# Optimization experiments

Hardware: AMD Instinct MI355X
Metric: run time of the kernel (lower is better)

## Reference

```python
import jax, jax.numpy as jnp
import numpy as np
from jax import lax

B = 16
DEPTH = 24
D_MODEL = 192
D_INNER = 384   # expand=2
D_STATE = 16
D_CONV = 4
DT_RANK = 12    # ceil(192/16)
PATCH = 16
EPS = 1e-5


def setup_inputs() -> dict:
    key = jax.random.key(0)
    ks = jax.random.split(key, 24)
    def n(k, shape, s):
        return jax.random.normal(k, shape, jnp.float32) * s
    inp = {}
    inp["x_img"] = jax.random.normal(ks[0], (B, 3, 256, 256), jnp.float32)
    inp["z_img"] = jax.random.normal(ks[1], (B, 3, 128, 128), jnp.float32)
    # patch embed conv
    inp["patch_w"] = n(ks[2], (D_MODEL, 3, PATCH, PATCH), 0.02)
    inp["patch_b"] = jnp.zeros((D_MODEL,), jnp.float32)
    # abs pos embeds (token counts fixed by module: 256 for x, 64 for z)
    inp["pos_x"] = n(ks[3], (1, 256, D_MODEL), 0.02)
    inp["pos_z"] = n(ks[4], (1, 64, D_MODEL), 0.02)
    # per-layer norms (LayerNorm, rms_norm=False)
    inp["ln_w"] = jnp.ones((DEPTH, D_MODEL), jnp.float32)
    inp["ln_b"] = jnp.zeros((DEPTH, D_MODEL), jnp.float32)
    # Mamba mixer params (stacked over depth)
    inp["in_w"] = n(ks[5], (DEPTH, 2 * D_INNER, D_MODEL), 0.05)          # in_proj (no bias)
    inp["conv_w"] = n(ks[6], (DEPTH, D_INNER, D_CONV), 0.2)              # depthwise conv1d
    inp["conv_b"] = jnp.zeros((DEPTH, D_INNER), jnp.float32)
    inp["xproj_w"] = n(ks[7], (DEPTH, DT_RANK + 2 * D_STATE, D_INNER), 0.05)  # x_proj (no bias)
    inp["dt_w"] = n(ks[8], (DEPTH, D_INNER, DT_RANK), 0.1)               # dt_proj weight
    # dt bias ~ inverse-softplus of dt in [1e-3, 0.1] (Mamba init)
    dt = jnp.exp(jax.random.uniform(ks[9], (DEPTH, D_INNER)) * (np.log(0.1) - np.log(1e-3)) + np.log(1e-3))
    inp["dt_b"] = dt + jnp.log(-jnp.expm1(-dt))
    # A_log init: log(1..d_state) per channel
    inp["A_log"] = jnp.log(jnp.tile(jnp.arange(1, D_STATE + 1, dtype=jnp.float32), (DEPTH, D_INNER, 1)))
    inp["D_skip"] = jnp.ones((DEPTH, D_INNER), jnp.float32)
    inp["out_w"] = n(ks[10], (DEPTH, D_MODEL, D_INNER), 0.05)            # out_proj (no bias)
    inp["fnorm_w"] = jnp.ones((D_MODEL,), jnp.float32)
    inp["fnorm_b"] = jnp.zeros((D_MODEL,), jnp.float32)
    return inp


def _layer_norm(x, w, b):
    mu = jnp.mean(x, axis=-1, keepdims=True)
    var = jnp.mean(jnp.square(x - mu), axis=-1, keepdims=True)
    return (x - mu) * lax.rsqrt(var + EPS) * w + b


def _patch_embed(img, w, b):
    # Conv2d stride=patch, then flatten HW -> tokens
    y = lax.conv_general_dilated(img, w, (PATCH, PATCH), 'VALID',
                                 dimension_numbers=('NCHW', 'OIHW', 'NCHW'))
    y = y + b[None, :, None, None]
    Bn, D, H, W = y.shape
    return y.reshape(Bn, D, H * W).transpose(0, 2, 1)  # (B, HW, D)


def _ssm_scan(dA, dBu):
    # h_t = dA_t * h_{t-1} + dBu_t, parallel over time via associative scan
    def comb(e1, e2):
        a1, b1 = e1
        a2, b2 = e2
        return a2 * a1, a2 * b1 + b2
    _, h = lax.associative_scan(comb, (dA, dBu), axis=1)
    return h  # (B, L, D_INNER, D_STATE)


def _mamba(h, in_w, conv_w, conv_b, xproj_w, dt_w, dt_b, A_log, D_skip, out_w):
    # h: (B, L, D_MODEL)
    xz = h @ in_w.T                                   # (B, L, 2*D_INNER)
    xc, zg = jnp.split(xz, 2, axis=-1)
    # causal depthwise conv over time
    xt = xc.transpose(0, 2, 1)                        # (B, D_INNER, L)
    xt = lax.conv_general_dilated(xt, conv_w[:, None, :], (1,), [(D_CONV - 1, 0)],
                                  feature_group_count=D_INNER,
                                  dimension_numbers=('NCH', 'OIH', 'NCH'))
    xt = xt + conv_b[None, :, None]
    xc = jax.nn.silu(xt).transpose(0, 2, 1)           # (B, L, D_INNER)
    dbl = xc @ xproj_w.T                              # (B, L, dt_rank + 2*d_state)
    dt, Bm, Cm = jnp.split(dbl, [DT_RANK, DT_RANK + D_STATE], axis=-1)
    dt = jax.nn.softplus(dt @ dt_w.T + dt_b)          # (B, L, D_INNER)
    A = -jnp.exp(A_log)                               # (D_INNER, D_STATE)
    dA = jnp.exp(dt[..., None] * A)                   # (B, L, D_INNER, D_STATE)
    dBu = dt[..., None] * Bm[:, :, None, :] * xc[..., None]
    hs = _ssm_scan(dA, dBu)
    y = jnp.einsum('bldn,bln->bld', hs, Cm) + xc * D_skip
    y = y * jax.nn.silu(zg)
    return y @ out_w.T                                # (B, L, D_MODEL)


def reference(x_img, z_img, patch_w, patch_b, pos_x, pos_z, ln_w, ln_b,
              in_w, conv_w, conv_b, xproj_w, dt_w, dt_b, A_log, D_skip,
              out_w, fnorm_w, fnorm_b):
    x_tok = _patch_embed(x_img, patch_w, patch_b) + pos_x   # (B, 256, D)
    z_tok = _patch_embed(z_img, patch_w, patch_b) + pos_z   # (B, 64, D)
    hidden = jnp.concatenate([z_tok, x_tok], axis=1)        # (B, 320, D)
    residual = None
    for i in range(DEPTH):
        # fused add-norm prenorm: residual = hidden + residual; hidden = LN(residual)
        residual = hidden if residual is None else hidden + residual
        h_n = _layer_norm(residual, ln_w[i], ln_b[i])
        hidden = _mamba(h_n, in_w[i], conv_w[i], conv_b[i], xproj_w[i],
                        dt_w[i], dt_b[i], A_log[i], D_skip[i], out_w[i])
    residual = residual + hidden
    return _layer_norm(residual, fnorm_w, fnorm_b)          # (B, 320, D), final_pool_type='none'
```

## Files before the change

### kernel.cpp

```cpp
#include <hip/hip_runtime.h>
#include <hip/hip_bf16.h>

#define BB 16
#define DEPTH 24
#define DM 192
#define DI 384
#define DS 16
#define DC 4
#define DTR 12
#define LL 320
#define NX 256
#define NZ 64
#define NT (BB * LL)
#define NC 10
#define LC 32
#define EPSV 1e-5f

__device__ inline float siluf(float x) { return x / (1.f + __expf(-x)); }
__device__ inline float softplusf(float x) {
    return (x > 20.f) ? x : log1pf(expf(x));
}
__device__ inline float wave_sum64(float v) {
    #pragma unroll
    for (int o = 32; o > 0; o >>= 1) v += __shfl_xor(v, o);
    return v;
}

__global__ __launch_bounds__(256) void addnorm_kernel(const float* hidden,
                                                      float* __restrict__ residual,
                                                      float* hn,
                                                      const float* __restrict__ w,
                                                      const float* __restrict__ bias,
                                                      size_t off, int first) {
    int t = blockIdx.x * 4 + (threadIdx.x >> 6);
    int lane = threadIdx.x & 63;
    size_t base = (size_t)t * DM;
    float a = hidden[base + lane];
    float b = hidden[base + 64 + lane];
    float c = hidden[base + 128 + lane];
    if (!first) {
        a += residual[base + lane];
        b += residual[base + 64 + lane];
        c += residual[base + 128 + lane];
    }
    residual[base + lane] = a;
    residual[base + 64 + lane] = b;
    residual[base + 128 + lane] = c;
    float mu = wave_sum64(a + b + c) * (1.f / 192.f);
    float va = a - mu, vb = b - mu, vc = c - mu;
    float var = wave_sum64(va * va + vb * vb + vc * vc) * (1.f / 192.f);
    float inv = rsqrtf(var + EPSV);
    hn[base + lane]       = va * inv * w[off + lane]       + bias[off + lane];
    hn[base + 64 + lane]  = vb * inv * w[off + 64 + lane]  + bias[off + 64 + lane];
    hn[base + 128 + lane] = vc * inv * w[off + 128 + lane] + bias[off + 128 + lane];
}

template<int K, int KT, int NO>
__global__ __launch_bounds__(256) void gemm_rt(const float* __restrict__ x,
                                               const float* __restrict__ w,
                                               size_t woff,
                                               float* __restrict__ out, int N) {
    constexpr int NCOL = 64 * NO;
    constexpr int KC = KT / 4;
    __shared__ float xs[32][KT + 4];
    __shared__ float ws[NCOL][KT + 4];
    int t0 = blockIdx.x * 32;
    int j0 = blockIdx.y * NCOL;
    int lane = threadIdx.x & 63;
    int wv = threadIdx.x >> 6;
    float acc[8][NO];
    #pragma unroll
    for (int t = 0; t < 8; t++)
        #pragma unroll
        for (int o = 0; o < NO; o++) acc[t][o] = 0.f;

    for (int kt = 0; kt < K; kt += KT) {
        for (int idx = threadIdx.x; idx < 32 * KC; idx += 256) {
            int tt = idx / KC, kc = idx % KC;
            float4 v = *(const float4*)&x[(size_t)(t0 + tt) * K + kt + kc * 4];
            *(float4*)&xs[tt][kc * 4] = v;
        }
        for (int idx = threadIdx.x; idx < NCOL * KC; idx += 256) {
            int jj = idx / KC, kc = idx % KC;
            float4 v = *(const float4*)&w[woff + (size_t)(j0 + jj) * K + kt + kc * 4];
            *(float4*)&ws[jj][kc * 4] = v;
        }
        __syncthreads();
        #pragma unroll 2
        for (int kk = 0; kk < KT; kk += 4) {
            float4 xv[8];
            #pragma unroll
            for (int t = 0; t < 8; t++)
                xv[t] = *(const float4*)&xs[wv * 8 + t][kk];
            #pragma unroll
            for (int o = 0; o < NO; o++) {
                float4 wv4 = *(const float4*)&ws[lane + 64 * o][kk];
                #pragma unroll
                for (int t = 0; t < 8; t++)
                    acc[t][o] += xv[t].x * wv4.x + xv[t].y * wv4.y
                               + xv[t].z * wv4.z + xv[t].w * wv4.w;
            }
        }
        __syncthreads();
    }
    #pragma unroll
    for (int t = 0; t < 8; t++)
        #pragma unroll
        for (int o = 0; o < NO; o++)
            out[(size_t)(t0 + wv * 8 + t) * N + j0 + lane + 64 * o] = acc[t][o];
}

__global__ __launch_bounds__(256) void patch_rt(const float* __restrict__ x_img,
                                                const float* __restrict__ z_img,
                                                const float* __restrict__ w,
                                                const float* __restrict__ bias,
                                                const float* __restrict__ pos_x,
                                                const float* __restrict__ pos_z,
                                                float* __restrict__ hidden) {
    __shared__ float xs[32][100];
    __shared__ float ws[64][100];
    bool isx = blockIdx.x < (BB * NX / 32);
    const float* img = isx ? x_img : z_img;
    const float* pos = isx ? pos_x : pos_z;
    int side = isx ? 16 : 8;
    int tok_off = isx ? NZ : 0;
    int ntok = side * side;
    int pt0 = (isx ? blockIdx.x : blockIdx.x - BB * NX / 32) * 32;
    int j0 = blockIdx.y * 64;
    int S = side * 16;
    int lane = threadIdx.x & 63;
    int wv = threadIdx.x >> 6;
    float acc[8];
    #pragma unroll
    for (int t = 0; t < 8; t++) acc[t] = 0.f;

    for (int kt = 0; kt < 768; kt += 96) {
        for (int idx = threadIdx.x; idx < 32 * 24; idx += 256) {
            int tt = idx / 24, kc = idx % 24;
            int k = kt + kc * 4;
            int c = k >> 8, p = k & 255, pi = p >> 4, pj = p & 15;
            int patch = pt0 + tt;
            int b = patch / ntok, t = patch % ntok;
            int ph = t / side, pw = t % side;
            float4 v = *(const float4*)&img[((size_t)(b * 3 + c) * S + ph * 16 + pi) * S
                                            + pw * 16 + pj];
            *(float4*)&xs[tt][kc * 4] = v;
        }
        for (int idx = threadIdx.x; idx < 64 * 24; idx += 256) {
            int jj = idx / 24, kc = idx % 24;
            float4 v = *(const float4*)&w[(size_t)(j0 + jj) * 768 + kt + kc * 4];
            *(float4*)&ws[jj][kc * 4] = v;
        }
        __syncthreads();
        #pragma unroll 2
        for (int kk = 0; kk < 96; kk += 4) {
            float4 xv[8];
            #pragma unroll
            for (int t = 0; t < 8; t++)
                xv[t] = *(const float4*)&xs[wv * 8 + t][kk];
            float4 wv4 = *(const float4*)&ws[lane][kk];
            #pragma unroll
            for (int t = 0; t < 8; t++)
                acc[t] += xv[t].x * wv4.x + xv[t].y * wv4.y
                        + xv[t].z * wv4.z + xv[t].w * wv4.w;
        }
        __syncthreads();
    }
    float bj = bias[j0 + lane];
    #pragma unroll
    for (int t = 0; t < 8; t++) {
        int patch = pt0 + wv * 8 + t;
        int b = patch / ntok, tk = patch % ntok;
        hidden[((size_t)b * LL + tok_off + tk) * DM + j0 + lane] =
            acc[t] + bj + pos[(size_t)tk * DM + j0 + lane];
    }
}

__global__ __launch_bounds__(256) void xpd_kernel(const float* __restrict__ xz,
                                                  const float* __restrict__ cw,
                                                  const float* __restrict__ cb,
                                                  const float* __restrict__ xpw,
                                                  const float* __restrict__ dtw,
                                                  const float* __restrict__ dtbias,
                                                  float* __restrict__ xc,
                                                  float* __restrict__ dbl,
                                                  float* __restrict__ dtbuf,
                                                  int layer) {
    __shared__ float smem[5760];
    float* xs   = smem;
    float* ws   = smem + 832;
    float* sdbl = smem;
    float* sdtw = smem + 768;

    int t0 = blockIdx.x * 16;
    int l0 = t0 % LL;
    int lane = threadIdx.x & 63;
    int wv = threadIdx.x >> 6;
    const float* cwl = cw  + (size_t)layer * DI * DC;
    const float* cbl = cb  + (size_t)layer * DI;
    const float* xpl = xpw + (size_t)layer * 44 * DI;
    float acc[4] = {0.f, 0.f, 0.f, 0.f};

    for (int kt = 0; kt < DI; kt += 48) {
        for (int idx = threadIdx.x; idx < 16 * 12; idx += 256) {
            int tt = idx / 12, kc = idx % 12;
            int d = kt + kc * 4;
            float4 a = *(const float4*)&cbl[d];
            float4 cw0 = *(const float4*)&cwl[(size_t)(d + 0) * 4];
            float4 cw1 = *(const float4*)&cwl[(size_t)(d + 1) * 4];
            float4 cw2 = *(const float4*)&cwl[(size_t)(d + 2) * 4];
            float4 cw3 = *(const float4*)&cwl[(size_t)(d + 3) * 4];
            const float* c0 = &cw0.x;
            const float* c1 = &cw1.x;
            const float* c2 = &cw2.x;
            const float* c3 = &cw3.x;
            #pragma unroll
            for (int rr = 0; rr < 4; rr++) {
                int l = l0 + tt - 3 + rr;
                float4 v = make_float4(0.f, 0.f, 0.f, 0.f);
                if (l >= 0)
                    v = *(const float4*)&xz[(size_t)(t0 + tt - 3 + rr) * 768 + d];
                a.x += c0[rr] * v.x;
                a.y += c1[rr] * v.y;
                a.z += c2[rr] * v.z;
                a.w += c3[rr] * v.w;
            }
            a.x = siluf(a.x); a.y = siluf(a.y); a.z = siluf(a.z); a.w = siluf(a.w);
            *(float4*)&xs[tt * 52 + kc * 4] = a;
            *(float4*)&xc[(size_t)(t0 + tt) * DI + d] = a;
        }
        for (int idx = threadIdx.x; idx < 64 * 12; idx += 256) {
            int jj = idx / 12, kc = idx % 12;
            float4 v = make_float4(0.f, 0.f, 0.f, 0.f);
            if (jj < 44)
                v = *(const float4*)&xpl[(size_t)jj * DI + kt + kc * 4];
            *(float4*)&ws[jj * 52 + kc * 4] = v;
        }
        __syncthreads();
        const float* wr0 = ws + lane * 52;
        #pragma unroll 4
        for (int kk = 0; kk < 48; kk += 4) {
            float4 xv0 = *(const float4*)&xs[(wv * 4 + 0) * 52 + kk];
            float4 xv1 = *(const float4*)&xs[(wv * 4 + 1) * 52 + kk];
            float4 xv2 = *(const float4*)&xs[(wv * 4 + 2) * 52 + kk];
            float4 xv3 = *(const float4*)&xs[(wv * 4 + 3) * 52 + kk];
            float4 wv4 = *(const float4*)&wr0[kk];
            acc[0] += xv0.x * wv4.x + xv0.y * wv4.y + xv0.z * wv4.z + xv0.w * wv4.w;
            acc[1] += xv1.x * wv4.x + xv1.y * wv4.y + xv1.z * wv4.z + xv1.w * wv4.w;
            acc[2] += xv2.x * wv4.x + xv2.y * wv4.y + xv2.z * wv4.z + xv2.w * wv4.w;
            acc[3] += xv3.x * wv4.x + xv3.y * wv4.y + xv3.z * wv4.z + xv3.w * wv4.w;
        }
        __syncthreads();
    }
    if (lane < 44) {
        #pragma unroll
        for (int t = 0; t < 4; t++) {
            sdbl[(wv * 4 + t) * 48 + lane] = acc[t];
            dbl[(size_t)(t0 + wv * 4 + t) * 44 + lane] = acc[t];
        }
    }
    const float* dwl = dtw + (size_t)layer * DI * DTR;
    for (int idx = threadIdx.x; idx < DI * DTR; idx += 256) {
        int d = idx / 12, rr = idx % 12;
        sdtw[d * 13 + rr] = dwl[idx];
    }
    __syncthreads();
    const float* dbb = dtbias + (size_t)layer * DI;
    for (int idx = threadIdx.x; idx < 16 * DI; idx += 256) {
        int tt = idx / DI, d = idx % DI;
        float a = dbb[d];
        const float* br = sdbl + tt * 48;
        const float* wr = sdtw + d * 13;
        #pragma unroll
        for (int rr = 0; rr < 12; rr++) a += br[rr] * wr[rr];
        dtbuf[(size_t)(t0 + tt) * DI + d] = softplusf(a);
    }
}

__global__ __launch_bounds__(320) void scan_fused(const float* __restrict__ dt,
                                                  const float* xc,
                                                  const float* __restrict__ dbl,
                                                  const float* __restrict__ xz,
                                                  const float* __restrict__ A_log,
                                                  const float* __restrict__ Dskip,
                                                  float* y,
                                                  size_t aoff, size_t doff) {
    __shared__ float sP[NC * 8 * 16];
    __shared__ float sH[NC * 8 * 16];
    int b = blockIdx.x / (DI / 8);
    int dbase = (blockIdx.x % (DI / 8)) * 8;
    int quad = threadIdx.x >> 2;
    int n0 = threadIdx.x & 3;
    int c = quad >> 3;
    int dl = quad & 7;
    int d = dbase + dl;
    float4 Al = *(const float4*)&A_log[aoff + (size_t)d * DS + n0 * 4];
    float A0 = -expf(Al.x), A1 = -expf(Al.y), A2 = -expf(Al.z), A3 = -expf(Al.w);
    int tbase = b * LL + c * LC;

    float h0 = 0.f, h1 = 0.f, h2 = 0.f, h3 = 0.f;
    float P0 = 1.f, P1 = 1.f, P2 = 1.f, P3 = 1.f;
    for (int l = 0; l < LC; l++) {
        size_t t = (size_t)tbase + l;
        float dtv = dt[t * DI + d];
        float xcv = xc[t * DI + d];
        float4 B4 = *(const float4*)&dbl[t * 44 + DTR + n0 * 4];
        float s = dtv * xcv;
        float e0 = __expf(dtv * A0), e1 = __expf(dtv * A1);
        float e2 = __expf(dtv * A2), e3 = __expf(dtv * A3);
        h0 = e0 * h0 + s * B4.x;  P0 *= e0;
        h1 = e1 * h1 + s * B4.y;  P1 *= e1;
        h2 = e2 * h2 + s * B4.z;  P2 *= e2;
        h3 = e3 * h3 + s * B4.w;  P3 *= e3;
    }
    int si = quad * 16 + n0 * 4;
    *(float4*)&sP[si] = make_float4(P0, P1, P2, P3);
    *(float4*)&sH[si] = make_float4(h0, h1, h2, h3);
    __syncthreads();

    h0 = h1 = h2 = h3 = 0.f;
    for (int cc = 0; cc < c; cc++) {
        int gi = (cc * 8 + dl) * 16 + n0 * 4;
        float4 P4 = *(const float4*)&sP[gi];
        float4 H4 = *(const float4*)&sH[gi];
        h0 = P4.x * h0 + H4.x;
        h1 = P4.y * h1 + H4.y;
        h2 = P4.z * h2 + H4.z;
        h3 = P4.w * h3 + H4.w;
    }

    float Dv = Dskip[doff + d];
    for (int l = 0; l < LC; l++) {
        size_t t = (size_t)tbase + l;
        float dtv = dt[t * DI + d];
        float xcv = xc[t * DI + d];
        float4 B4 = *(const float4*)&dbl[t * 44 + DTR + n0 * 4];
        float4 C4 = *(const float4*)&dbl[t * 44 + DTR + DS + n0 * 4];
        float s = dtv * xcv;
        float e0 = __expf(dtv * A0), e1 = __expf(dtv * A1);
        float e2 = __expf(dtv * A2), e3 = __expf(dtv * A3);
        h0 = e0 * h0 + s * B4.x;
        h1 = e1 * h1 + s * B4.y;
        h2 = e2 * h2 + s * B4.z;
        h3 = e3 * h3 + s * B4.w;
        float p = h0 * C4.x + h1 * C4.y + h2 * C4.z + h3 * C4.w;
        p += __shfl_xor(p, 1);
        p += __shfl_xor(p, 2);
        if (n0 == 0) {
            float zg = xz[t * (2 * DI) + DI + d];
            y[t * DI + d] = (p + xcv * Dv) * siluf(zg);
        }
    }
}

__global__ __launch_bounds__(256) void final_kernel(const float* __restrict__ hidden,
                                                    const float* __restrict__ residual,
                                                    const float* __restrict__ w,
                                                    const float* __restrict__ bias,
                                                    float* __restrict__ out) {
    int t = blockIdx.x * 4 + (threadIdx.x >> 6);
    int lane = threadIdx.x & 63;
    size_t base = (size_t)t * DM;
    float a = residual[base + lane]       + hidden[base + lane];
    float b = residual[base + 64 + lane]  + hidden[base + 64 + lane];
    float c = residual[base + 128 + lane] + hidden[base + 128 + lane];
    float mu = wave_sum64(a + b + c) * (1.f / 192.f);
    float va = a - mu, vb = b - mu, vc = c - mu;
    float var = wave_sum64(va * va + vb * vb + vc * vc) * (1.f / 192.f);
    float inv = rsqrtf(var + EPSV);
    out[base + lane]       = va * inv * w[lane]       + bias[lane];
    out[base + 64 + lane]  = vb * inv * w[64 + lane]  + bias[64 + lane];
    out[base + 128 + lane] = vc * inv * w[128 + lane] + bias[128 + lane];
}

extern "C" void kernel_launch(void* const* d_in, const int* in_sizes, int n_in,
                              void* d_out, int out_size, void* d_ws, size_t ws_size,
                              hipStream_t stream) {
    const float* x_img   = (const float*)d_in[0];
    const float* z_img   = (const float*)d_in[1];
    const float* patch_w = (const float*)d_in[2];
    const float* patch_b = (const float*)d_in[3];
    const float* pos_x   = (const float*)d_in[4];
    const float* pos_z   = (const float*)d_in[5];
    const float* ln_w    = (const float*)d_in[6];
    const float* ln_b    = (const float*)d_in[7];
    const float* in_w    = (const float*)d_in[8];
    const float* conv_w  = (const float*)d_in[9];
    const float* conv_b  = (const float*)d_in[10];
    const float* xproj_w = (const float*)d_in[11];
    const float* dt_w    = (const float*)d_in[12];
    const float* dt_b    = (const float*)d_in[13];
    const float* A_log   = (const float*)d_in[14];
    const float* D_skip  = (const float*)d_in[15];
    const float* out_w   = (const float*)d_in[16];
    const float* fnorm_w = (const float*)d_in[17];
    const float* fnorm_b = (const float*)d_in[18];

    float* hidden   = (float*)d_ws;
    float* residual = hidden   + (size_t)NT * DM;
    float* xz       = residual + (size_t)NT * DM;
    float* xc       = xz       + (size_t)NT * 2 * DI;
    float* dbl      = xc       + (size_t)NT * DI;
    float* dtbuf    = dbl      + (size_t)NT * 44;
    float* hn       = hidden;
    float* yb       = xc;

    {
        dim3 gp((BB * NX + BB * NZ) / 32, 3);
        patch_rt<<<gp, 256, 0, stream>>>(x_img, z_img, patch_w, patch_b,
                                         pos_x, pos_z, hidden);
    }

    const int scan_blocks = BB * (DI / 8);
    for (int i = 0; i < DEPTH; i++) {
        addnorm_kernel<<<NT / 4, 256, 0, stream>>>(
            hidden, residual, hn, ln_w, ln_b, (size_t)i * DM, i == 0 ? 1 : 0);
        {
            dim3 g(NT / 32, 3);
            gemm_rt<192, 24, 4><<<g, 256, 0, stream>>>(
                hn, in_w, (size_t)i * 768 * 192, xz, 768);
        }
        xpd_kernel<<<NT / 16, 256, 0, stream>>>(
            xz, conv_w, conv_b, xproj_w, dt_w, dt_b, xc, dbl, dtbuf, i);
        scan_fused<<<scan_blocks, 320, 0, stream>>>(
            dtbuf, xc, dbl, xz, A_log, D_skip, yb,
            (size_t)i * DI * DS, (size_t)i * DI);
        {
            dim3 g(NT / 32, 3);
            gemm_rt<384, 96, 1><<<g, 256, 0, stream>>>(
                yb, out_w, (size_t)i * 192 * 384, hidden, 192);
        }
    }

    final_kernel<<<NT / 4, 256, 0, stream>>>(hidden, residual, fnorm_w, fnorm_b,
                                             (float*)d_out);
}
```

Measured before the change: 3.946 ms.

## Fuse out_proj GEMM with residual add and next layer's LayerNorm

Replaces the out_proj GEMM and the separate add-norm kernel with one kernel that computes the GEMM for 16 tokens, covering all 192 output columns per block. It then adds the residual and applies the next layer's LayerNorm, or the final norm on the last layer. This removes one launch per layer and the write and re-read of the hidden buffer. In exchange the grid shrinks to 320 blocks, each loading the whole weight slice, which may lower parallelism and increase redundant weight traffic compared with the old 3-way column-split GEMM.

Result: slower. 4.255 ms (+7.8%).

```diff
diff --git a/kernel.cpp b/kernel.cpp
--- a/kernel.cpp
+++ b/kernel.cpp
@@ -31,18 +31,13 @@
                                                       float* hn,
                                                       const float* __restrict__ w,
                                                       const float* __restrict__ bias,
-                                                      size_t off, int first) {
+                                                      size_t off) {
     int t = blockIdx.x * 4 + (threadIdx.x >> 6);
     int lane = threadIdx.x & 63;
     size_t base = (size_t)t * DM;
     float a = hidden[base + lane];
     float b = hidden[base + 64 + lane];
     float c = hidden[base + 128 + lane];
-    if (!first) {
-        a += residual[base + lane];
-        b += residual[base + 64 + lane];
-        c += residual[base + 128 + lane];
-    }
     residual[base + lane] = a;
     residual[base + 64 + lane] = b;
     residual[base + 128 + lane] = c;
@@ -108,6 +103,75 @@
         #pragma unroll
         for (int o = 0; o < NO; o++)
             out[(size_t)(t0 + wv * 8 + t) * N + j0 + lane + 64 * o] = acc[t][o];
+}
+
+__global__ __launch_bounds__(256) void gemm_out_ln(const float* __restrict__ y,
+                                                   const float* __restrict__ w,
+                                                   size_t woff,
+                                                   float* __restrict__ residual,
+                                                   float* __restrict__ hn,
+                                                   const float* __restrict__ lnw,
+                                                   const float* __restrict__ lnb,
+                                                   size_t lnoff, int last) {
+    __shared__ float xs[16][52];
+    __shared__ float ws[192][52];
+    int t0 = blockIdx.x * 16;
+    int lane = threadIdx.x & 63;
+    int wv = threadIdx.x >> 6;
+    float acc[4][3];
+    #pragma unroll
+    for (int t = 0; t < 4; t++)
+        #pragma unroll
+        for (int o = 0; o < 3; o++) acc[t][o] = 0.f;
+
+    for (int kt = 0; kt < 384; kt += 48) {
+        for (int idx = threadIdx.x; idx < 16 * 12; idx += 256) {
+            int tt = idx / 12, kc = idx % 12;
+            *(float4*)&xs[tt][kc * 4] =
+                *(const float4*)&y[(size_t)(t0 + tt) * 384 + kt + kc * 4];
+        }
+        for (int idx = threadIdx.x; idx < 192 * 12; idx += 256) {
+            int jj = idx / 12, kc = idx % 12;
+            *(float4*)&ws[jj][kc * 4] =
+                *(const float4*)&w[woff + (size_t)jj * 384 + kt + kc * 4];
+        }
+        __syncthreads();
+        #pragma unroll 2
+        for (int kk = 0; kk < 48; kk += 4) {
+            float4 xv[4];
+            #pragma unroll
+            for (int t = 0; t < 4; t++)
+                xv[t] = *(const float4*)&xs[wv * 4 + t][kk];
+            #pragma unroll
+            for (int o = 0; o < 3; o++) {
+                float4 wv4 = *(const float4*)&ws[lane + 64 * o][kk];
+                #pragma unroll
+                for (int t = 0; t < 4; t++)
+                    acc[t][o] += xv[t].x * wv4.x + xv[t].y * wv4.y
+                               + xv[t].z * wv4.z + xv[t].w * wv4.w;
+            }
+        }
+        __syncthreads();
+    }
+    #pragma unroll
+    for (int t = 0; t < 4; t++) {
+        size_t base = (size_t)(t0 + wv * 4 + t) * DM;
+        float a = acc[t][0] + residual[base + lane];
+        float b = acc[t][1] + residual[base + 64 + lane];
+        float c = acc[t][2] + residual[base + 128 + lane];
+        if (!last) {
+            residual[base + lane]       = a;
+            residual[base + 64 + lane]  = b;
+            residual[base + 128 + lane] = c;
+        }
+        float mu = wave_sum64(a + b + c) * (1.f / 192.f);
+        float va = a - mu, vb = b - mu, vc = c - mu;
+        float var = wave_sum64(va * va + vb * vb + vc * vc) * (1.f / 192.f);
+        float inv = rsqrtf(var + EPSV);
+        hn[base + lane]       = va * inv * lnw[lnoff + lane]       + lnb[lnoff + lane];
+        hn[base + 64 + lane]  = vb * inv * lnw[lnoff + 64 + lane]  + lnb[lnoff + 64 + lane];
+        hn[base + 128 + lane] = vc * inv * lnw[lnoff + 128 + lane] + lnb[lnoff + 128 + lane];
+    }
 }
 
 __global__ __launch_bounds__(256) void patch_rt(const float* __restrict__ x_img,
@@ -351,26 +415,6 @@
             y[t * DI + d] = (p + xcv * Dv) * siluf(zg);
         }
     }
-}
-
-__global__ __launch_bounds__(256) void final_kernel(const float* __restrict__ hidden,
-                                                    const float* __restrict__ residual,
-                                                    const float* __restrict__ w,
-                                                    const float* __restrict__ bias,
-                                                    float* __restrict__ out) {
-    int t = blockIdx.x * 4 + (threadIdx.x >> 6);
-    int lane = threadIdx.x & 63;
-    size_t base = (size_t)t * DM;
-    float a = residual[base + lane]       + hidden[base + lane];
-    float b = residual[base + 64 + lane]  + hidden[base + 64 + lane];
-    float c = residual[base + 128 + lane] + hidden[base + 128 + lane];
-    float mu = wave_sum64(a + b + c) * (1.f / 192.f);
-    float va = a - mu, vb = b - mu, vc = c - mu;
-    float var = wave_sum64(va * va + vb * vb + vc * vc) * (1.f / 192.f);
-    float inv = rsqrtf(var + EPSV);
-    out[base + lane]       = va * inv * w[lane]       + bias[lane];
-    out[base + 64 + lane]  = vb * inv * w[64 + lane]  + bias[64 + lane];
-    out[base + 128 + lane] = vc * inv * w[128 + lane] + bias[128 + lane];
 }
 
 extern "C" void kernel_launch(void* const* d_in, const int* in_sizes, int n_in,
@@ -411,10 +455,11 @@
                                          pos_x, pos_z, hidden);
     }
 
+    addnorm_kernel<<<NT / 4, 256, 0, stream>>>(
+        hidden, residual, hn, ln_w, ln_b, 0);
+
     const int scan_blocks = BB * (DI / 8);
     for (int i = 0; i < DEPTH; i++) {
-        addnorm_kernel<<<NT / 4, 256, 0, stream>>>(
-            hidden, residual, hn, ln_w, ln_b, (size_t)i * DM, i == 0 ? 1 : 0);
         {
             dim3 g(NT / 32, 3);
             gemm_rt<192, 24, 4><<<g, 256, 0, stream>>>(
@@ -425,13 +470,14 @@
         scan_fused<<<scan_blocks, 320, 0, stream>>>(
             dtbuf, xc, dbl, xz, A_log, D_skip, yb,
             (size_t)i * DI * DS, (size_t)i * DI);
-        {
-            dim3 g(NT / 32, 3);
-            gemm_rt<384, 96, 1><<<g, 256, 0, stream>>>(
-                yb, out_w, (size_t)i * 192 * 384, hidden, 192);
-        }
-    }
-
-    final_kernel<<<NT / 4, 256, 0, stream>>>(hidden, residual, fnorm_w, fnorm_b,
-                                             (float*)d_out);
-}
+        if (i < DEPTH - 1) {
+            gemm_out_ln<<<NT / 16, 256, 0, stream>>>(
+                yb, out_w, (size_t)i * 192 * 384, residual, hn,
+                ln_w, ln_b, (size_t)(i + 1) * DM, 0);
+        } else {
+            gemm_out_ln<<<NT / 16, 256, 0, stream>>>(
+                yb, out_w, (size_t)i * 192 * 384, residual, (float*)d_out,
+                fnorm_w, fnorm_b, 0, 1);
+        }
+    }
+}
```
